# Optimization experiments

Measured on AMD Instinct MI355X. Metric: run time of the kernel, lower is better.

Reference implementation:

```python
import jax, jax.numpy as jnp
import numpy as np

B, T, N, C = 1, 8, 1152, 768
H, DH = 12, 64          # attention heads / head dim; also RG-LRU block-diagonal heads
MLP = 3072
LRU = 768
CONV_W = 4              # recurrentgemma temporal conv width
N_IMG = 1024            # image tokens blocked by mask_image2image


def rms_norm(x, scale):
    var = jnp.mean(jnp.square(x), axis=-1, keepdims=True)
    return x * jax.lax.rsqrt(var + 1e-6) * (1.0 + scale)


def layer_norm(x, scale, bias):
    m = jnp.mean(x, axis=-1, keepdims=True)
    v = jnp.var(x, axis=-1, keepdims=True)
    return (x - m) * jax.lax.rsqrt(v + 1e-6) * scale + bias


def block_diag_linear(x, w, b):
    # x [..., LRU] -> per-head block-diagonal linear (recurrentgemma BlockDiagonalLinear)
    xs = x.reshape(x.shape[:-1] + (H, DH))
    y = jnp.einsum('...hd,hde->...he', xs, w) + b
    return y.reshape(x.shape)


def setup_inputs():
    key = jax.random.key(0)
    ks = jax.random.split(key, 24)
    def nrm(k, shape, s=0.02):
        return jax.random.normal(k, shape, jnp.float32) * s
    return dict(
        x=jax.random.normal(ks[0], (B, T, N, C), jnp.float32),
        tpre_scale=nrm(ks[1], (C,)),
        w_y=nrm(ks[2], (C, LRU)), b_y=jnp.zeros((LRU,)),
        w_x=nrm(ks[3], (C, LRU)), b_x=jnp.zeros((LRU,)),
        conv_w=nrm(ks[4], (CONV_W, LRU)), conv_b=jnp.zeros((LRU,)),
        a_param=jax.random.uniform(ks[5], (LRU,), jnp.float32, 1.0, 4.0),
        ig_w=nrm(ks[6], (H, DH, DH)), ig_b=jnp.zeros((H, DH)),
        ag_w=nrm(ks[7], (H, DH, DH)), ag_b=jnp.zeros((H, DH)),
        w_out=nrm(ks[8], (LRU, C)), b_out=jnp.zeros((C,)),
        cpre_scale=nrm(ks[9], (C,)),
        ffw_up_w=nrm(ks[10], (2, C, MLP)), ffw_up_b=jnp.zeros((2, MLP)),
        ffw_down_w=nrm(ks[11], (MLP, C)), ffw_down_b=jnp.zeros((C,)),
        ln1_s=jnp.ones((C,)), ln1_b=jnp.zeros((C,)),
        wq=nrm(ks[12], (C, H, DH)), bq=jnp.zeros((H, DH)),
        wk=nrm(ks[13], (C, H, DH)), bk=jnp.zeros((H, DH)),
        wv=nrm(ks[14], (C, H, DH)), bv=jnp.zeros((H, DH)),
        wo=nrm(ks[15], (H, DH, C)), bo=jnp.zeros((C,)),
        ln2_s=jnp.ones((C,)), ln2_b=jnp.zeros((C,)),
        mlp_w1=nrm(ks[16], (C, MLP)), mlp_b1=jnp.zeros((MLP,)),
        mlp_w2=nrm(ks[17], (MLP, C)), mlp_b2=jnp.zeros((C,)),
    )


def forward(x, tpre_scale, w_y, b_y, w_x, b_x, conv_w, conv_b, a_param,
            ig_w, ig_b, ag_w, ag_b, w_out, b_out, cpre_scale,
            ffw_up_w, ffw_up_b, ffw_down_w, ffw_down_b,
            ln1_s, ln1_b, wq, bq, wk, bk, wv, bv, wo, bo,
            ln2_s, ln2_b, mlp_w1, mlp_b1, mlp_w2, mlp_b2):
    b, t, n, c = x.shape
    # ---- temporal RG-LRU residual block over time: [(b t) n c] -> [(b n) t c] ----
    xt = x.transpose(0, 2, 1, 3).reshape(b * n, t, c)
    raw = xt
    xn = rms_norm(xt, tpre_scale)
    y = jax.nn.gelu(xn @ w_y + b_y)              # gate branch
    u = xn @ w_x + b_x                           # recurrent branch
    # causal depthwise temporal conv (width 4)
    up = jnp.pad(u, ((0, 0), (CONV_W - 1, 0), (0, 0)))
    u = sum(conv_w[i] * up[:, i:i + t] for i in range(CONV_W)) + conv_b
    # RG-LRU
    gate_x = jax.nn.sigmoid(block_diag_linear(u, ig_w, ig_b))
    gate_a = jax.nn.sigmoid(block_diag_linear(u, ag_w, ag_b))
    log_a = -8.0 * gate_a * jax.nn.softplus(a_param)
    a = jnp.exp(log_a)                           # [bn, t, LRU]
    mult = jnp.sqrt(jnp.maximum(1.0 - jnp.exp(2.0 * log_a), 0.0))
    reset = (jnp.arange(t) == 0)[None, :, None]
    mult = jnp.where(reset, 1.0, mult)
    a = jnp.where(reset, 0.0, a)
    norm_x = u * gate_x * mult
    def step(h, inputs):
        a_t, x_t = inputs
        h = a_t * h + x_t
        return h, h
    _, hs = jax.lax.scan(step, jnp.zeros((b * n, LRU), u.dtype),
                         (a.transpose(1, 0, 2), norm_x.transpose(1, 0, 2)))
    h = hs.transpose(1, 0, 2)                    # [bn, t, LRU]
    s = (h * y) @ w_out + b_out
    resid = s + raw
    # gated MLP (recurrentgemma MLPBlock)
    z = rms_norm(resid, cpre_scale)
    up2 = jnp.einsum('btd,cdD->cbtD', z, ffw_up_w) + ffw_up_b[:, None, None, :]
    z = (jax.nn.gelu(up2[0]) * up2[1]) @ ffw_down_w + ffw_down_b
    xt = z + resid
    # ---- spatial ViT block over tokens: back to [(b t) n c] ----
    xs = xt.reshape(b, n, t, c).transpose(0, 2, 1, 3).reshape(b * t, n, c)
    y1 = layer_norm(xs, ln1_s, ln1_b)
    q = jnp.einsum('bnc,chd->bnhd', y1, wq) + bq
    k = jnp.einsum('bnc,chd->bnhd', y1, wk) + bk
    v = jnp.einsum('bnc,chd->bnhd', y1, wv) + bv
    logits = jnp.einsum('bqhd,bkhd->bhqk', q, k) / jnp.sqrt(jnp.asarray(DH, q.dtype))
    # mask_image2image: image tokens (first 1024) cannot attend to image tokens
    mask = jnp.ones((n, n), bool).at[:N_IMG, :N_IMG].set(False)
    logits = jnp.where(mask[None, None], logits, jnp.finfo(logits.dtype).min)
    attn = jax.nn.softmax(logits, axis=-1)
    sa = jnp.einsum('bhqk,bkhd->bqhd', attn, v)
    sa = jnp.einsum('bqhd,hdc->bqc', sa, wo) + bo
    xs = xs + sa
    y2 = layer_norm(xs, ln2_s, ln2_b)
    m = jax.nn.gelu(y2 @ mlp_w1 + mlp_b1) @ mlp_w2 + mlp_b2
    xs = xs + m
    return xs.reshape(b, t, n, c)


def reference(x, tpre_scale, w_y, b_y, w_x, b_x, conv_w, conv_b, a_param,
              ig_w, ig_b, ag_w, ag_b, w_out, b_out, cpre_scale,
              ffw_up_w, ffw_up_b, ffw_down_w, ffw_down_b,
              ln1_s, ln1_b, wq, bq, wk, bk, wv, bv, wo, bo,
              ln2_s, ln2_b, mlp_w1, mlp_b1, mlp_w2, mlp_b2):
    return forward(x, tpre_scale, w_y, b_y, w_x, b_x, conv_w, conv_b, a_param,
                   ig_w, ig_b, ag_w, ag_b, w_out, b_out, cpre_scale,
                   ffw_up_w, ffw_up_b, ffw_down_w, ffw_down_b,
                   ln1_s, ln1_b, wq, bq, wk, bk, wv, bv, wo, bo,
                   ln2_s, ln2_b, mlp_w1, mlp_b1, mlp_w2, mlp_b2)
```

## Files before the change

kernel.cpp:

```cpp
#include <hip/hip_runtime.h>
#include <hip/hip_bf16.h>

typedef __hip_bfloat16 bf16;
typedef __attribute__((ext_vector_type(4))) float f32x4;
typedef __attribute__((ext_vector_type(8))) short short8;

#define T_ 8
#define N_ 1152
#define C_ 768
#define H_ 12
#define DH_ 64
#define MLP_ 3072
#define LRU_ 768
#define NIMG_ 1024
#define M_ (T_*N_)

__device__ __forceinline__ float b2f(bf16 v){ return __bfloat162float(v); }
__device__ __forceinline__ bf16  f2b(float f){ return __float2bfloat16(f); }
__device__ __forceinline__ float gelu_tanh(float x){
  float x3 = x*x*x;
  float z = 1.5957691216057308f*(x + 0.044715f*x3);
  float e = __expf(z);
  float t = 1.f - 2.f/(e + 1.f);
  return 0.5f*x*(1.f + t);
}
__device__ __forceinline__ void gll16(const void* g, void* l) {
  __builtin_amdgcn_global_load_lds((const __attribute__((address_space(1))) void*)g,
                                   (__attribute__((address_space(3))) void*)l, 16, 0, 0);
}
__device__ __forceinline__ f32x4 mfma16(short8 a, short8 b, f32x4 c) {
  return __builtin_amdgcn_mfma_f32_16x16x32_bf16(a, b, c, 0, 0, 0);
}

__global__ __launch_bounds__(256)
void convertT(const float* __restrict__ W, bf16* __restrict__ Wt, int Kd, int Nd,
              int rs, int ro) {
  __shared__ float tile[64][65];
  int k0 = blockIdx.y * 64, n0 = blockIdx.x * 64;
  int tid = threadIdx.x;
  int c = tid & 63, rr = tid >> 6;
  #pragma unroll
  for (int i = 0; i < 16; i++) {
    int r = rr * 16 + i;
    tile[r][c] = W[(size_t)(k0 + r) * Nd + n0 + c];
  }
  __syncthreads();
  #pragma unroll
  for (int i = 0; i < 16; i++) {
    int n = rr * 16 + i;
    Wt[(size_t)((n0 + n) * rs + ro) * Kd + k0 + c] = f2b(tile[c][n]);
  }
}

__global__ __launch_bounds__(256)
void convert_gw(const float* __restrict__ igw, const float* __restrict__ agw,
                const float* __restrict__ igb, const float* __restrict__ agb,
                bf16* __restrict__ GW, float* __restrict__ GB) {
  int h = blockIdx.x;
  for (int idx = threadIdx.x; idx < 128 * 64; idx += 256) {
    int rowc = idx >> 6;
    int d    = idx & 63;
    int e    = rowc >> 1;
    const float* W = (rowc & 1) ? agw : igw;
    GW[((size_t)h * 128 + rowc) * 64 + d] = f2b(W[((size_t)h * 64 + d) * 64 + e]);
  }
  if (threadIdx.x < 128) {
    int rowc = threadIdx.x;
    GB[h * 128 + rowc] = ((rowc & 1) ? agb : igb)[h * 64 + (rowc >> 1)];
  }
}

template<int EPI, int ACT>
__global__ __launch_bounds__(256)
void mgemm(const bf16* __restrict__ A, const bf16* __restrict__ Wt,
           const float* __restrict__ bias, const float* __restrict__ resid,
           void* __restrict__ outp, int K, int Nd) {
  __shared__ bf16 As[2][128][32];
  __shared__ bf16 Bs[2][128][32];
  int tid = threadIdx.x;
  int wave = tid >> 6, lane = tid & 63;
  int wm = wave >> 1, wn = wave & 1;
  int ln15 = lane & 15, quad = lane >> 4;
  int row0 = blockIdx.y * 128, col0 = blockIdx.x * 128;
  const bf16* ag = A  + (size_t)(row0 + wave*32 + (lane>>2)) * K + (lane&3)*8;
  const bf16* bg = Wt + (size_t)(col0 + wave*32 + (lane>>2)) * K + (lane&3)*8;
  f32x4 zero = {0.f, 0.f, 0.f, 0.f};
  f32x4 acc[4][4];
  #pragma unroll
  for (int i = 0; i < 4; i++)
    #pragma unroll
    for (int j = 0; j < 4; j++) acc[i][j] = zero;

  gll16(ag,          &As[0][wave*32][0]);
  gll16(ag + 16*K,   &As[0][wave*32 + 16][0]);
  gll16(bg,          &Bs[0][wave*32][0]);
  gll16(bg + 16*K,   &Bs[0][wave*32 + 16][0]);
  __syncthreads();

  int nt = K >> 5;
  int cur = 0;
  for (int t = 0; t < nt; ++t) {
    if (t + 1 < nt) {
      int k1 = (t + 1) << 5;
      gll16(ag + k1,          &As[cur^1][wave*32][0]);
      gll16(ag + 16*K + k1,   &As[cur^1][wave*32 + 16][0]);
      gll16(bg + k1,          &Bs[cur^1][wave*32][0]);
      gll16(bg + 16*K + k1,   &Bs[cur^1][wave*32 + 16][0]);
    }
    short8 af[4], bf[4];
    #pragma unroll
    for (int i = 0; i < 4; i++)
      af[i] = *(const short8*)&As[cur][wm*64 + i*16 + ln15][quad*8];
    #pragma unroll
    for (int i = 0; i < 4; i++)
      bf[i] = *(const short8*)&Bs[cur][wn*64 + i*16 + ln15][quad*8];
    #pragma unroll
    for (int i = 0; i < 4; i++)
      #pragma unroll
      for (int j = 0; j < 4; j++)
        acc[i][j] = mfma16(af[i], bf[j], acc[i][j]);
    __syncthreads();
    cur ^= 1;
  }

  #pragma unroll
  for (int i = 0; i < 4; i++) {
    #pragma unroll
    for (int j = 0; j < 4; j++) {
      int col = col0 + wn*64 + j*16 + ln15;
      float bv = (EPI == 3) ? bias[(col & 1) * (Nd >> 1) + (col >> 1)] : bias[col];
      #pragma unroll
      for (int r = 0; r < 4; r++) {
        int row = row0 + wm*64 + i*16 + quad*4 + r;
        float v = acc[i][j][r] + bv;
        if (EPI == 3) {
          float pv = __shfl_xor(v, 1, 64);
          if ((lane & 1) == 0)
            ((bf16*)outp)[(size_t)row * (Nd >> 1) + (col >> 1)] = f2b(gelu_tanh(v) * pv);
        } else {
          if (ACT) v = gelu_tanh(v);
          if (EPI == 0) {
            ((bf16*)outp)[(size_t)row * Nd + col] = f2b(v);
          } else if (EPI == 1) {
            size_t o = (size_t)row * Nd + col;
            ((float*)outp)[o] = v + resid[o];
          } else if (EPI == 2) {
            int tt = row / N_; int nn = row - tt * N_;
            ((bf16*)outp)[(((size_t)tt * H_ + (col >> 6)) * 64 + (col & 63)) * N_ + nn] = f2b(v);
          }
        }
      }
    }
  }
}

template<int LN>
__global__ __launch_bounds__(256)
void norm_kernel(const float* __restrict__ inp, const float* __restrict__ s,
                 const float* __restrict__ b, bf16* __restrict__ out) {
  int wid  = threadIdx.x >> 6;
  int lane = threadIdx.x & 63;
  int tok  = blockIdx.x * 4 + wid;
  float v[12];
  float sum = 0.f, sq = 0.f;
  #pragma unroll
  for (int i = 0; i < 12; i++) {
    int c = lane + i * 64;
    float x = inp[(size_t)tok*C_ + c];
    v[i] = x; sum += x; sq += x * x;
  }
  #pragma unroll
  for (int o = 32; o > 0; o >>= 1) {
    sum += __shfl_xor(sum, o, 64);
    sq  += __shfl_xor(sq, o, 64);
  }
  float scale, mean = 0.f;
  if (LN) {
    mean = sum * (1.f / C_);
    float var = sq * (1.f / C_) - mean * mean;
    scale = rsqrtf(var + 1e-6f);
  } else {
    scale = rsqrtf(sq * (1.f / C_) + 1e-6f);
  }
  #pragma unroll
  for (int i = 0; i < 12; i++) {
    int c = lane + i * 64;
    float sc = s[c];
    float r;
    if (LN) r = (v[i] - mean) * scale * sc + b[c];
    else    r = v[i] * scale * (1.f + sc);
    out[(size_t)tok*C_ + c] = f2b(r);
  }
}

__global__ __launch_bounds__(256)
void conv_kernel(const bf16* __restrict__ u0, const float* __restrict__ cw,
                 const float* __restrict__ cb, bf16* __restrict__ uc) {
  int idx = blockIdx.x * 256 + threadIdx.x;
  int ch  = idx % LRU_;
  int tok = idx / LRU_;
  int n = tok % N_;
  int t = tok / N_;
  float acc = cb[ch];
  #pragma unroll
  for (int i = 0; i < 4; i++) {
    int tt = t - 3 + i;
    if (tt >= 0)
      acc += cw[i*LRU_ + ch] * b2f(u0[(size_t)(tt*N_ + n)*LRU_ + ch]);
  }
  uc[idx] = f2b(acc);
}

__global__ __launch_bounds__(256)
void gates_mfma(const bf16* __restrict__ uc, const bf16* __restrict__ GW,
                const float* __restrict__ GB, const float* __restrict__ ap,
                bf16* __restrict__ a_out, bf16* __restrict__ nx_out) {
  __shared__ bf16 As[128][64];
  __shared__ bf16 Bs[128][64];
  int tid = threadIdx.x;
  int wave = tid >> 6, lane = tid & 63;
  int wm = wave >> 1, wn = wave & 1;
  int ln15 = lane & 15, quad = lane >> 4;
  int row0 = blockIdx.x * 128;
  int h = blockIdx.y;
  #pragma unroll
  for (int i = 0; i < 4; i++) {
    int chunk = wave * 4 + i;
    gll16(uc + (size_t)(row0 + chunk*8 + (lane>>3)) * LRU_ + h*DH_ + (lane&7)*8,
          &As[chunk*8][0]);
    gll16(GW + (size_t)h*128*64 + chunk*512 + lane*8, &Bs[chunk*8][0]);
  }
  __syncthreads();
  f32x4 zero = {0.f, 0.f, 0.f, 0.f};
  f32x4 acc[4][4];
  #pragma unroll
  for (int i = 0; i < 4; i++)
    #pragma unroll
    for (int j = 0; j < 4; j++) acc[i][j] = zero;
  short8 af0[4], af1[4], bf0[4], bf1[4];
  #pragma unroll
  for (int i = 0; i < 4; i++) {
    af0[i] = *(const short8*)&As[wm*64 + i*16 + ln15][quad*8];
    af1[i] = *(const short8*)&As[wm*64 + i*16 + ln15][32 + quad*8];
    bf0[i] = *(const short8*)&Bs[wn*64 + i*16 + ln15][quad*8];
    bf1[i] = *(const short8*)&Bs[wn*64 + i*16 + ln15][32 + quad*8];
  }
  #pragma unroll
  for (int i = 0; i < 4; i++)
    #pragma unroll
    for (int j = 0; j < 4; j++) {
      acc[i][j] = mfma16(af0[i], bf0[j], acc[i][j]);
      acc[i][j] = mfma16(af1[i], bf1[j], acc[i][j]);
    }
  __syncthreads();

  int t_is0 = (row0 < N_);
  int odd = lane & 1;
  float bvj[4], spj[4];
  #pragma unroll
  for (int j = 0; j < 4; j++) {
    int col = wn*64 + j*16 + ln15;
    bvj[j] = GB[h*128 + col];
    int e = col >> 1;
    float apv = ap[h*DH_ + e];
    spj[j] = (apv > 20.f) ? apv : log1pf(__expf(apv));
  }
  #pragma unroll
  for (int i = 0; i < 4; i++) {
    #pragma unroll
    for (int j = 0; j < 4; j++) {
      int col = wn*64 + j*16 + ln15;
      int e = col >> 1;
      #pragma unroll
      for (int r = 0; r < 4; r++) {
        int lr = wm*64 + i*16 + quad*4 + r;
        float v = acc[i][j][r] + bvj[j];
        float g = 1.f / (1.f + __expf(-v));
        float mult = 1.f;
        if (odd) {
          float log_a = -8.f * g * spj[j];
          float a = __expf(log_a);
          mult = sqrtf(fmaxf(1.f - a*a, 0.f));
          if (t_is0) { a = 0.f; mult = 1.f; }
          Bs[lr][e] = f2b(a);
        }
        float mp = __shfl_xor(mult, 1, 64);
        if (!odd) {
          float uv = b2f(As[lr][e]);
          As[lr][e] = f2b(uv * g * mp);
        }
      }
    }
  }
  __syncthreads();
  int rr = tid >> 3, cc = (tid & 7) * 8;
  #pragma unroll
  for (int it = 0; it < 4; it++) {
    int row = it * 32 + rr;
    size_t o = (size_t)(row0 + row) * LRU_ + h*DH_ + cc;
    *(short8*)(nx_out + o) = *(const short8*)&As[row][cc];
    *(short8*)(a_out  + o) = *(const short8*)&Bs[row][cc];
  }
}

__global__ __launch_bounds__(256)
void scan_kernel(const bf16* __restrict__ a, const bf16* __restrict__ nx,
                 const bf16* __restrict__ y, bf16* __restrict__ hy) {
  int idx = blockIdx.x * 256 + threadIdx.x;
  int n  = idx / LRU_;
  int ch = idx % LRU_;
  float h = 0.f;
  #pragma unroll
  for (int t = 0; t < T_; t++) {
    size_t p = (size_t)(t*N_ + n) * LRU_ + ch;
    h = b2f(a[p]) * h + b2f(nx[p]);
    hy[p] = f2b(h * b2f(y[p]));
  }
}

__global__ __launch_bounds__(256)
void fattn(const bf16* __restrict__ Q, const bf16* __restrict__ Kg,
           const bf16* __restrict__ Vt, bf16* __restrict__ O) {
  __shared__ bf16 Ks[128][64];
  __shared__ bf16 VTs[64][128];
  __shared__ bf16 Ps[4][16][128];
  int qb = blockIdx.x, th = blockIdx.y;
  int h = th % H_, t = th / H_;
  int wave = threadIdx.x >> 6, lane = threadIdx.x & 63;
  int ln15 = lane & 15, quad = lane >> 4;
  int q0, kv0, nch;
  if (qb < 16) { q0 = qb * 64;            kv0 = NIMG_; nch = 1; }
  else         { q0 = NIMG_ + (qb-16)*64; kv0 = 0;     nch = 9; }
  int qw = q0 + wave * 16;
  const bf16* qp = Q + (size_t)(t*N_ + qw + ln15) * C_ + h*DH_ + quad*8;
  short8 aq0 = *(const short8*)qp;
  short8 aq1 = *(const short8*)(qp + 32);
  f32x4 zero = {0.f, 0.f, 0.f, 0.f};
  f32x4 oacc[4];
  #pragma unroll
  for (int d = 0; d < 4; d++) oacc[d] = zero;
  float mi[4], li[4];
  #pragma unroll
  for (int r = 0; r < 4; r++) { mi[r] = -1e30f; li[r] = 0.f; }

  for (int ch = 0; ch < nch; ch++) {
    int kb = t*N_ + kv0 + ch*128;
    #pragma unroll
    for (int i = 0; i < 4; i++) {
      int r = wave*32 + i*8;
      gll16(Kg + (size_t)(kb + r + (lane>>3))*C_ + h*DH_ + (lane&7)*8, &Ks[r][0]);
    }
    #pragma unroll
    for (int i = 0; i < 4; i++) {
      int d = wave*16 + i*4;
      gll16(Vt + ((size_t)(t*H_ + h)*64 + d + (lane>>4))*N_ + kv0 + ch*128 + ln15*8,
            &VTs[d][0]);
    }
    __syncthreads();
    f32x4 s[8];
    #pragma unroll
    for (int nt = 0; nt < 8; nt++) {
      short8 b0 = *(const short8*)&Ks[nt*16 + ln15][quad*8];
      short8 b1 = *(const short8*)&Ks[nt*16 + ln15][32 + quad*8];
      f32x4 c_ = zero;
      c_ = mfma16(aq0, b0, c_);
      c_ = mfma16(aq1, b1, c_);
      #pragma unroll
      for (int r = 0; r < 4; r++) s[nt][r] = c_[r] * 0.125f;
    }
    float alpha[4], lsum[4];
    #pragma unroll
    for (int r = 0; r < 4; r++) {
      float m_ = s[0][r];
      #pragma unroll
      for (int nt = 1; nt < 8; nt++) m_ = fmaxf(m_, s[nt][r]);
      #pragma unroll
      for (int o = 1; o < 16; o <<= 1) m_ = fmaxf(m_, __shfl_xor(m_, o, 64));
      float mnew = fmaxf(mi[r], m_);
      alpha[r] = __expf(mi[r] - mnew);
      mi[r] = mnew;
      lsum[r] = 0.f;
    }
    #pragma unroll
    for (int nt = 0; nt < 8; nt++)
      #pragma unroll
      for (int r = 0; r < 4; r++) {
        float p = __expf(s[nt][r] - mi[r]);
        s[nt][r] = p; lsum[r] += p;
      }
    #pragma unroll
    for (int r = 0; r < 4; r++) {
      float l_ = lsum[r];
      #pragma unroll
      for (int o = 1; o < 16; o <<= 1) l_ += __shfl_xor(l_, o, 64);
      li[r] = li[r] * alpha[r] + l_;
    }
    #pragma unroll
    for (int nt = 0; nt < 8; nt++)
      #pragma unroll
      for (int r = 0; r < 4; r++)
        Ps[wave][quad*4 + r][nt*16 + ln15] = f2b(s[nt][r]);
    #pragma unroll
    for (int d = 0; d < 4; d++)
      #pragma unroll
      for (int r = 0; r < 4; r++) oacc[d][r] *= alpha[r];
    #pragma unroll
    for (int ks = 0; ks < 4; ks++) {
      short8 pa = *(const short8*)&Ps[wave][ln15][ks*32 + quad*8];
      #pragma unroll
      for (int dt = 0; dt < 4; dt++) {
        short8 vb = *(const short8*)&VTs[dt*16 + ln15][ks*32 + quad*8];
        oacc[dt] = mfma16(pa, vb, oacc[dt]);
      }
    }
    __syncthreads();
  }
  #pragma unroll
  for (int dt = 0; dt < 4; dt++)
    #pragma unroll
    for (int r = 0; r < 4; r++)
      O[(size_t)(t*N_ + qw + quad*4 + r)*C_ + h*DH_ + dt*16 + ln15]
        = f2b(oacc[dt][r] / li[r]);
}

extern "C" void kernel_launch(void* const* d_in, const int* in_sizes, int n_in,
                              void* d_out, int out_size, void* d_ws, size_t ws_size,
                              hipStream_t stream) {
  (void)in_sizes; (void)n_in; (void)out_size; (void)ws_size;
  const float* x        = (const float*)d_in[0];
  const float* tpre     = (const float*)d_in[1];
  const float* w_y      = (const float*)d_in[2];
  const float* b_y      = (const float*)d_in[3];
  const float* w_x      = (const float*)d_in[4];
  const float* b_x      = (const float*)d_in[5];
  const float* conv_w   = (const float*)d_in[6];
  const float* conv_b   = (const float*)d_in[7];
  const float* a_param  = (const float*)d_in[8];
  const float* ig_w     = (const float*)d_in[9];
  const float* ig_b     = (const float*)d_in[10];
  const float* ag_w     = (const float*)d_in[11];
  const float* ag_b     = (const float*)d_in[12];
  const float* w_out    = (const float*)d_in[13];
  const float* b_out    = (const float*)d_in[14];
  const float* cpre     = (const float*)d_in[15];
  const float* ffw_up_w = (const float*)d_in[16];
  const float* ffw_up_b = (const float*)d_in[17];
  const float* ffw_dn_w = (const float*)d_in[18];
  const float* ffw_dn_b = (const float*)d_in[19];
  const float* ln1_s    = (const float*)d_in[20];
  const float* ln1_b    = (const float*)d_in[21];
  const float* wq       = (const float*)d_in[22];
  const float* bq       = (const float*)d_in[23];
  const float* wk       = (const float*)d_in[24];
  const float* bk       = (const float*)d_in[25];
  const float* wv       = (const float*)d_in[26];
  const float* bv       = (const float*)d_in[27];
  const float* wo       = (const float*)d_in[28];
  const float* bo       = (const float*)d_in[29];
  const float* ln2_s    = (const float*)d_in[30];
  const float* ln2_b    = (const float*)d_in[31];
  const float* mlp_w1   = (const float*)d_in[32];
  const float* mlp_b1   = (const float*)d_in[33];
  const float* mlp_w2   = (const float*)d_in[34];
  const float* mlp_b2   = (const float*)d_in[35];

  const size_t MC = (size_t)M_ * C_;
  const size_t W68 = (size_t)C_ * C_;
  const size_t WUP = (size_t)C_ * MLP_;
  bf16* B0 = (bf16*)d_ws;
  bf16* B1 = B0 + MC;
  bf16* B2 = B1 + MC;
  bf16* BV = B2 + MC;
  float* F0 = (float*)(BV + MC);
  float* F1 = F0 + MC;
  bf16* F0b = (bf16*)F0;
  bf16* B0b = (bf16*)B0;
  float* xsF = (float*)B0;
  float* outF = (float*)d_out;
  bf16*  GW = (bf16*)F1;
  float* GB = (float*)(GW + (size_t)H_*128*64);

  dim3 blk(256);
  dim3 gN768(C_/128, M_/128);
  dim3 cv768(12, 12);
  dim3 cvUp(48, 12);
  dim3 cvDn(12, 48);

  convertT<<<cv768, blk, 0, stream>>>(w_y, BV, C_, C_, 1, 0);
  convertT<<<cv768, blk, 0, stream>>>(w_x, BV + W68, C_, C_, 1, 0);
  convert_gw<<<H_, blk, 0, stream>>>(ig_w, ag_w, ig_b, ag_b, GW, GB);
  norm_kernel<0><<<M_/4, blk, 0, stream>>>(x, tpre, nullptr, B0);
  mgemm<0,1><<<gN768, blk, 0, stream>>>(B0, BV, b_y, nullptr, B1, C_, C_);
  mgemm<0,0><<<gN768, blk, 0, stream>>>(B0, BV + W68, b_x, nullptr, B2, C_, C_);
  conv_kernel<<<(M_*LRU_)/256, blk, 0, stream>>>(B2, conv_w, conv_b, B0);
  gates_mfma<<<dim3(M_/128, H_), blk, 0, stream>>>(B0, GW, GB, a_param, B2, BV);
  scan_kernel<<<(N_*LRU_)/256, blk, 0, stream>>>(B2, BV, B1, B0);
  convertT<<<cv768, blk, 0, stream>>>(w_out, BV, C_, C_, 1, 0);
  mgemm<1,0><<<gN768, blk, 0, stream>>>(B0, BV, b_out, x, outF, C_, C_);

  norm_kernel<0><<<M_/4, blk, 0, stream>>>(outF, cpre, nullptr, B0);
  convertT<<<cvUp, blk, 0, stream>>>(ffw_up_w,       B1, C_, MLP_, 2, 0);
  convertT<<<cvUp, blk, 0, stream>>>(ffw_up_w + WUP, B1, C_, MLP_, 2, 1);
  convertT<<<cvDn, blk, 0, stream>>>(ffw_dn_w, BV, MLP_, C_, 1, 0);
  {
    dim3 gUp(6144/128, M_/128);
    dim3 gDn(C_/128,   M_/128);
    mgemm<3,0><<<gUp, blk, 0, stream>>>(B0, B1, ffw_up_b, nullptr, F0b, C_, 6144);
    mgemm<1,0><<<gDn, blk, 0, stream>>>(F0b, BV, ffw_dn_b, outF, xsF, MLP_, C_);
  }

  norm_kernel<1><<<M_/4, blk, 0, stream>>>(xsF, ln1_s, ln1_b, B2);
  convertT<<<cv768, blk, 0, stream>>>(wq, BV,          C_, C_, 1, 0);
  convertT<<<cv768, blk, 0, stream>>>(wk, BV + W68,    C_, C_, 1, 0);
  convertT<<<cv768, blk, 0, stream>>>(wv, BV + 2*W68,  C_, C_, 1, 0);
  convertT<<<cv768, blk, 0, stream>>>(wo, BV + 3*W68,  C_, C_, 1, 0);
  mgemm<0,0><<<gN768, blk, 0, stream>>>(B2, BV,         bq, nullptr, F0b,        C_, C_);
  mgemm<0,0><<<gN768, blk, 0, stream>>>(B2, BV + W68,   bk, nullptr, F0b + MC,   C_, C_);
  mgemm<2,0><<<gN768, blk, 0, stream>>>(B2, BV + 2*W68, bv, nullptr, F0b + 2*MC, C_, C_);
  fattn<<<dim3(18, T_*H_), blk, 0, stream>>>(F0b, F0b + MC, F0b + 2*MC, B2);
  mgemm<1,0><<<gN768, blk, 0, stream>>>(B2, BV + 3*W68, bo, xsF, outF, C_, C_);
  norm_kernel<1><<<M_/4, blk, 0, stream>>>(outF, ln2_s, ln2_b, B2);
  convertT<<<cvUp, blk, 0, stream>>>(mlp_w1, B0b,       C_, MLP_, 1, 0);
  convertT<<<cvDn, blk, 0, stream>>>(mlp_w2, B0b + WUP, MLP_, C_, 1, 0);
  {
    dim3 gM1(MLP_/128, M_/128);
    dim3 gM2(C_/128,   M_/128);
    mgemm<0,1><<<gM1, blk, 0, stream>>>(B2, B0b, mlp_b1, nullptr, F0b, C_, MLP_);
    mgemm<1,0><<<gM2, blk, 0, stream>>>(F0b, B0b + WUP, mlp_b2, outF, outF, MLP_, C_);
  }
}
```

Baseline: 928.6 us.

## Merge y/x and Q/K projection GEMMs; make K compile-time with unrolled double-buffer

The y and x projections of the recurrent block become one GEMM with a 1536-wide output, and so do the Q and K projections of attention. An epilogue mode applies the split bias and a GELU on the first half only. Downstream kernels (conv, scan, flash attention) now read the interleaved 1536-stride buffers. The GEMM also takes K as a template parameter and unrolls the double-buffered loop by two, which removes the buffer-index arithmetic. Together these cut kernel launches and give larger grids, at the cost of strided reads in the consumer kernels.

```diff
diff --git a/kernel.cpp b/kernel.cpp
--- a/kernel.cpp
+++ b/kernel.cpp
@@ -70,13 +70,14 @@
   }
 }
 
-template<int EPI, int ACT>
+template<int EPI, int ACT, int K>
 __global__ __launch_bounds__(256)
 void mgemm(const bf16* __restrict__ A, const bf16* __restrict__ Wt,
-           const float* __restrict__ bias, const float* __restrict__ resid,
-           void* __restrict__ outp, int K, int Nd) {
+           const float* __restrict__ bias, const float* __restrict__ bias2,
+           void* __restrict__ outp, int Nd) {
   __shared__ bf16 As[2][128][32];
   __shared__ bf16 Bs[2][128][32];
+  constexpr int NT = K >> 5;
   int tid = threadIdx.x;
   int wave = tid >> 6, lane = tid & 63;
   int wm = wave >> 1, wn = wave & 1;
@@ -91,36 +92,37 @@
     #pragma unroll
     for (int j = 0; j < 4; j++) acc[i][j] = zero;
 
-  gll16(ag,          &As[0][wave*32][0]);
-  gll16(ag + 16*K,   &As[0][wave*32 + 16][0]);
-  gll16(bg,          &Bs[0][wave*32][0]);
-  gll16(bg + 16*K,   &Bs[0][wave*32 + 16][0]);
+  auto stage = [&](int kt, int buf) {
+    int kk = kt << 5;
+    gll16(ag + kk,          &As[buf][wave*32][0]);
+    gll16(ag + 16*K + kk,   &As[buf][wave*32 + 16][0]);
+    gll16(bg + kk,          &Bs[buf][wave*32][0]);
+    gll16(bg + 16*K + kk,   &Bs[buf][wave*32 + 16][0]);
+  };
+  auto compute = [&](int buf) {
+    short8 af[4], bf_[4];
+    #pragma unroll
+    for (int i = 0; i < 4; i++)
+      af[i] = *(const short8*)&As[buf][wm*64 + i*16 + ln15][quad*8];
+    #pragma unroll
+    for (int i = 0; i < 4; i++)
+      bf_[i] = *(const short8*)&Bs[buf][wn*64 + i*16 + ln15][quad*8];
+    #pragma unroll
+    for (int i = 0; i < 4; i++)
+      #pragma unroll
+      for (int j = 0; j < 4; j++)
+        acc[i][j] = mfma16(af[i], bf_[j], acc[i][j]);
+  };
+
+  stage(0, 0);
   __syncthreads();
-
-  int nt = K >> 5;
-  int cur = 0;
-  for (int t = 0; t < nt; ++t) {
-    if (t + 1 < nt) {
-      int k1 = (t + 1) << 5;
-      gll16(ag + k1,          &As[cur^1][wave*32][0]);
-      gll16(ag + 16*K + k1,   &As[cur^1][wave*32 + 16][0]);
-      gll16(bg + k1,          &Bs[cur^1][wave*32][0]);
-      gll16(bg + 16*K + k1,   &Bs[cur^1][wave*32 + 16][0]);
-    }
-    short8 af[4], bf[4];
-    #pragma unroll
-    for (int i = 0; i < 4; i++)
-      af[i] = *(const short8*)&As[cur][wm*64 + i*16 + ln15][quad*8];
-    #pragma unroll
-    for (int i = 0; i < 4; i++)
-      bf[i] = *(const short8*)&Bs[cur][wn*64 + i*16 + ln15][quad*8];
-    #pragma unroll
-    for (int i = 0; i < 4; i++)
-      #pragma unroll
-      for (int j = 0; j < 4; j++)
-        acc[i][j] = mfma16(af[i], bf[j], acc[i][j]);
+  for (int t = 0; t < NT; t += 2) {
+    stage(t + 1, 1);
+    compute(0);
     __syncthreads();
-    cur ^= 1;
+    if (t + 2 < NT) stage(t + 2, 0);
+    compute(1);
+    __syncthreads();
   }
 
   #pragma unroll
@@ -128,7 +130,10 @@
     #pragma unroll
     for (int j = 0; j < 4; j++) {
       int col = col0 + wn*64 + j*16 + ln15;
-      float bv = (EPI == 3) ? bias[(col & 1) * (Nd >> 1) + (col >> 1)] : bias[col];
+      float bv;
+      if (EPI == 3)      bv = bias[(col & 1) * (Nd >> 1) + (col >> 1)];
+      else if (EPI == 4) bv = (col < (Nd >> 1)) ? bias[col] : bias2[col - (Nd >> 1)];
+      else               bv = bias[col];
       #pragma unroll
       for (int r = 0; r < 4; r++) {
         int row = row0 + wm*64 + i*16 + quad*4 + r;
@@ -137,13 +142,16 @@
           float pv = __shfl_xor(v, 1, 64);
           if ((lane & 1) == 0)
             ((bf16*)outp)[(size_t)row * (Nd >> 1) + (col >> 1)] = f2b(gelu_tanh(v) * pv);
+        } else if (EPI == 4) {
+          if (ACT && col < (Nd >> 1)) v = gelu_tanh(v);
+          ((bf16*)outp)[(size_t)row * Nd + col] = f2b(v);
         } else {
           if (ACT) v = gelu_tanh(v);
           if (EPI == 0) {
             ((bf16*)outp)[(size_t)row * Nd + col] = f2b(v);
           } else if (EPI == 1) {
             size_t o = (size_t)row * Nd + col;
-            ((float*)outp)[o] = v + resid[o];
+            ((float*)outp)[o] = v + bias2[o];
           } else if (EPI == 2) {
             int tt = row / N_; int nn = row - tt * N_;
             ((bf16*)outp)[(((size_t)tt * H_ + (col >> 6)) * 64 + (col & 63)) * N_ + nn] = f2b(v);
@@ -195,7 +203,7 @@
 
 __global__ __launch_bounds__(256)
 void conv_kernel(const bf16* __restrict__ u0, const float* __restrict__ cw,
-                 const float* __restrict__ cb, bf16* __restrict__ uc) {
+                 const float* __restrict__ cb, bf16* __restrict__ uc, int us, int uo) {
   int idx = blockIdx.x * 256 + threadIdx.x;
   int ch  = idx % LRU_;
   int tok = idx / LRU_;
@@ -206,7 +214,7 @@
   for (int i = 0; i < 4; i++) {
     int tt = t - 3 + i;
     if (tt >= 0)
-      acc += cw[i*LRU_ + ch] * b2f(u0[(size_t)(tt*N_ + n)*LRU_ + ch]);
+      acc += cw[i*LRU_ + ch] * b2f(u0[(size_t)(tt*N_ + n)*us + uo + ch]);
   }
   uc[idx] = f2b(acc);
 }
@@ -305,7 +313,7 @@
 
 __global__ __launch_bounds__(256)
 void scan_kernel(const bf16* __restrict__ a, const bf16* __restrict__ nx,
-                 const bf16* __restrict__ y, bf16* __restrict__ hy) {
+                 const bf16* __restrict__ y, bf16* __restrict__ hy, int ys) {
   int idx = blockIdx.x * 256 + threadIdx.x;
   int n  = idx / LRU_;
   int ch = idx % LRU_;
@@ -314,13 +322,13 @@
   for (int t = 0; t < T_; t++) {
     size_t p = (size_t)(t*N_ + n) * LRU_ + ch;
     h = b2f(a[p]) * h + b2f(nx[p]);
-    hy[p] = f2b(h * b2f(y[p]));
-  }
-}
-
-__global__ __launch_bounds__(256)
-void fattn(const bf16* __restrict__ Q, const bf16* __restrict__ Kg,
-           const bf16* __restrict__ Vt, bf16* __restrict__ O) {
+    hy[p] = f2b(h * b2f(y[(size_t)(t*N_ + n) * ys + ch]));
+  }
+}
+
+__global__ __launch_bounds__(256)
+void fattn(const bf16* __restrict__ QK, const bf16* __restrict__ Vt,
+           bf16* __restrict__ O) {
   __shared__ bf16 Ks[128][64];
   __shared__ bf16 VTs[64][128];
   __shared__ bf16 Ps[4][16][128];
@@ -332,7 +340,7 @@
   if (qb < 16) { q0 = qb * 64;            kv0 = NIMG_; nch = 1; }
   else         { q0 = NIMG_ + (qb-16)*64; kv0 = 0;     nch = 9; }
   int qw = q0 + wave * 16;
-  const bf16* qp = Q + (size_t)(t*N_ + qw + ln15) * C_ + h*DH_ + quad*8;
+  const bf16* qp = QK + (size_t)(t*N_ + qw + ln15) * 1536 + h*DH_ + quad*8;
   short8 aq0 = *(const short8*)qp;
   short8 aq1 = *(const short8*)(qp + 32);
   f32x4 zero = {0.f, 0.f, 0.f, 0.f};
@@ -348,7 +356,7 @@
     #pragma unroll
     for (int i = 0; i < 4; i++) {
       int r = wave*32 + i*8;
-      gll16(Kg + (size_t)(kb + r + (lane>>3))*C_ + h*DH_ + (lane&7)*8, &Ks[r][0]);
+      gll16(QK + (size_t)(kb + r + (lane>>3))*1536 + 768 + h*DH_ + (lane&7)*8, &Ks[r][0]);
     }
     #pragma unroll
     for (int i = 0; i < 4; i++) {
@@ -482,6 +490,7 @@
 
   dim3 blk(256);
   dim3 gN768(C_/128, M_/128);
+  dim3 g1536(1536/128, M_/128);
   dim3 cv768(12, 12);
   dim3 cvUp(48, 12);
   dim3 cvDn(12, 48);
@@ -490,13 +499,12 @@
   convertT<<<cv768, blk, 0, stream>>>(w_x, BV + W68, C_, C_, 1, 0);
   convert_gw<<<H_, blk, 0, stream>>>(ig_w, ag_w, ig_b, ag_b, GW, GB);
   norm_kernel<0><<<M_/4, blk, 0, stream>>>(x, tpre, nullptr, B0);
-  mgemm<0,1><<<gN768, blk, 0, stream>>>(B0, BV, b_y, nullptr, B1, C_, C_);
-  mgemm<0,0><<<gN768, blk, 0, stream>>>(B0, BV + W68, b_x, nullptr, B2, C_, C_);
-  conv_kernel<<<(M_*LRU_)/256, blk, 0, stream>>>(B2, conv_w, conv_b, B0);
-  gates_mfma<<<dim3(M_/128, H_), blk, 0, stream>>>(B0, GW, GB, a_param, B2, BV);
-  scan_kernel<<<(N_*LRU_)/256, blk, 0, stream>>>(B2, BV, B1, B0);
+  mgemm<4,1,C_><<<g1536, blk, 0, stream>>>(B0, BV, b_y, b_x, F0b, 1536);
+  conv_kernel<<<(M_*LRU_)/256, blk, 0, stream>>>(F0b, conv_w, conv_b, B1, 1536, 768);
+  gates_mfma<<<dim3(M_/128, H_), blk, 0, stream>>>(B1, GW, GB, a_param, B2, BV);
+  scan_kernel<<<(N_*LRU_)/256, blk, 0, stream>>>(B2, BV, F0b, B0, 1536);
   convertT<<<cv768, blk, 0, stream>>>(w_out, BV, C_, C_, 1, 0);
-  mgemm<1,0><<<gN768, blk, 0, stream>>>(B0, BV, b_out, x, outF, C_, C_);
+  mgemm<1,0,C_><<<gN768, blk, 0, stream>>>(B0, BV, b_out, x, outF, C_);
 
   norm_kernel<0><<<M_/4, blk, 0, stream>>>(outF, cpre, nullptr, B0);
   convertT<<<cvUp, blk, 0, stream>>>(ffw_up_w,       B1, C_, MLP_, 2, 0);
@@ -505,8 +513,8 @@
   {
     dim3 gUp(6144/128, M_/128);
     dim3 gDn(C_/128,   M_/128);
-    mgemm<3,0><<<gUp, blk, 0, stream>>>(B0, B1, ffw_up_b, nullptr, F0b, C_, 6144);
-    mgemm<1,0><<<gDn, blk, 0, stream>>>(F0b, BV, ffw_dn_b, outF, xsF, MLP_, C_);
+    mgemm<3,0,C_><<<gUp, blk, 0, stream>>>(B0, B1, ffw_up_b, nullptr, F0b, 6144);
+    mgemm<1,0,MLP_><<<gDn, blk, 0, stream>>>(F0b, BV, ffw_dn_b, outF, xsF, C_);
   }
 
   norm_kernel<1><<<M_/4, blk, 0, stream>>>(xsF, ln1_s, ln1_b, B2);
@@ -514,18 +522,17 @@
   convertT<<<cv768, blk, 0, stream>>>(wk, BV + W68,    C_, C_, 1, 0);
   convertT<<<cv768, blk, 0, stream>>>(wv, BV + 2*W68,  C_, C_, 1, 0);
   convertT<<<cv768, blk, 0, stream>>>(wo, BV + 3*W68,  C_, C_, 1, 0);
-  mgemm<0,0><<<gN768, blk, 0, stream>>>(B2, BV,         bq, nullptr, F0b,        C_, C_);
-  mgemm<0,0><<<gN768, blk, 0, stream>>>(B2, BV + W68,   bk, nullptr, F0b + MC,   C_, C_);
-  mgemm<2,0><<<gN768, blk, 0, stream>>>(B2, BV + 2*W68, bv, nullptr, F0b + 2*MC, C_, C_);
-  fattn<<<dim3(18, T_*H_), blk, 0, stream>>>(F0b, F0b + MC, F0b + 2*MC, B2);
-  mgemm<1,0><<<gN768, blk, 0, stream>>>(B2, BV + 3*W68, bo, xsF, outF, C_, C_);
+  mgemm<4,0,C_><<<g1536, blk, 0, stream>>>(B2, BV, bq, bk, F0b, 1536);
+  mgemm<2,0,C_><<<gN768, blk, 0, stream>>>(B2, BV + 2*W68, bv, nullptr, F0b + 2*MC, C_);
+  fattn<<<dim3(18, T_*H_), blk, 0, stream>>>(F0b, F0b + 2*MC, B2);
+  mgemm<1,0,C_><<<gN768, blk, 0, stream>>>(B2, BV + 3*W68, bo, xsF, outF, C_);
   norm_kernel<1><<<M_/4, blk, 0, stream>>>(outF, ln2_s, ln2_b, B2);
   convertT<<<cvUp, blk, 0, stream>>>(mlp_w1, B0b,       C_, MLP_, 1, 0);
   convertT<<<cvDn, blk, 0, stream>>>(mlp_w2, B0b + WUP, MLP_, C_, 1, 0);
   {
     dim3 gM1(MLP_/128, M_/128);
     dim3 gM2(C_/128,   M_/128);
-    mgemm<0,1><<<gM1, blk, 0, stream>>>(B2, B0b, mlp_b1, nullptr, F0b, C_, MLP_);
-    mgemm<1,0><<<gM2, blk, 0, stream>>>(F0b, B0b + WUP, mlp_b2, outF, outF, MLP_, C_);
-  }
-}
+    mgemm<0,1,C_><<<gM1, blk, 0, stream>>>(B2, B0b, mlp_b1, nullptr, F0b, MLP_);
+    mgemm<1,0,MLP_><<<gM2, blk, 0, stream>>>(F0b, B0b + WUP, mlp_b2, outF, outF, C_);
+  }
+}
```

New measurement: 935.5 us. About the same (+0.7%).
